# Kernel tuning notes

Measured on AMD Instinct MI355X. Metric: run time of the kernel, lower is better.

The kernel has to match this reference:

```python
import jax, jax.numpy as jnp
import numpy as np

C = 192          # filter_channels (= in_channels in this module)
K = 3            # kernel_size
NB = 10          # num_bins of rational-quadratic spline (VITS default)
TB = 5.0         # tail_bound
NF = 4           # number of ConvFlow steps per branch
L = 3            # DDSConv n_layers
LOG2PI = float(np.log(2.0 * np.pi))


def conv1x1(x, w, b):
    # x: (B, Cin, T), w: (Cout, Cin)
    return jnp.einsum('oi,bit->bot', w, x) + b[None, :, None]


def depthwise(x, w, b, dil):
    # x: (B, C, T), w: (C, 1, K), dilated depthwise conv, 'same' padding
    pad = dil * (K - 1) // 2
    y = jax.lax.conv_general_dilated(
        x, w, window_strides=(1,), padding=[(pad, pad)], rhs_dilation=(dil,),
        dimension_numbers=('NCH', 'OIH', 'NCH'), feature_group_count=x.shape[1])
    return y + b[None, :, None]


def layer_norm_c(x, g, b, eps=1e-5):
    # VITS LayerNorm: normalize over the channel axis (axis=1)
    m = jnp.mean(x, axis=1, keepdims=True)
    v = jnp.mean((x - m) ** 2, axis=1, keepdims=True)
    return (x - m) * jax.lax.rsqrt(v + eps) * g[None, :, None] + b[None, :, None]


def dds(x, x_mask, g, dep_w, dep_b, pw_w, pw_b, ln_g, ln_b):
    # DDSConv: dilated depth-separable conv stack with residual
    if g is not None:
        x = x + g
    for i in range(L):
        dil = K ** i
        y = depthwise(x * x_mask, dep_w[i], dep_b[i], dil)
        y = jax.nn.gelu(layer_norm_c(y, ln_g[i, 0], ln_b[i, 0]))
        y = conv1x1(y, pw_w[i], pw_b[i])
        y = jax.nn.gelu(layer_norm_c(y, ln_g[i, 1], ln_b[i, 1]))
        x = x + y  # dropout disabled in deterministic reference
    return x * x_mask


def ew_affine(z, x_mask, m, logs):
    y = (m[None, :, None] + jnp.exp(logs)[None, :, None] * z) * x_mask
    ld = jnp.sum(logs[None, :, None] * x_mask, axis=(1, 2))
    return y, ld


def rqs_forward(x_in, uw, uh, ud):
    # unconstrained rational-quadratic spline, forward direction, linear tails
    mb = 1e-3  # min bin width / height / derivative
    const = float(np.log(np.expm1(1.0 - mb)))
    inside = (x_in >= -TB) & (x_in <= TB)
    ud = jnp.pad(ud, ((0, 0), (0, 0), (0, 0), (1, 1)), constant_values=const)
    wd = jax.nn.softmax(uw, -1); wd = mb + (1.0 - mb * NB) * wd
    cw = jnp.cumsum(wd, -1)
    cw = jnp.concatenate([jnp.zeros_like(cw[..., :1]), cw], -1)
    cw = 2.0 * TB * cw - TB
    cw = cw.at[..., 0].set(-TB).at[..., -1].set(TB)
    wd = cw[..., 1:] - cw[..., :-1]
    ht = jax.nn.softmax(uh, -1); ht = mb + (1.0 - mb * NB) * ht
    ch = jnp.cumsum(ht, -1)
    ch = jnp.concatenate([jnp.zeros_like(ch[..., :1]), ch], -1)
    ch = 2.0 * TB * ch - TB
    ch = ch.at[..., 0].set(-TB).at[..., -1].set(TB)
    ht = ch[..., 1:] - ch[..., :-1]
    dv = mb + jax.nn.softplus(ud)  # (..., NB+1)
    xc = jnp.clip(x_in, -TB, TB)
    idx = jnp.clip(jnp.sum((xc[..., None] >= cw[..., :-1]).astype(jnp.int32), -1) - 1, 0, NB - 1)
    g = lambda a, i: jnp.take_along_axis(a, i[..., None], -1)[..., 0]
    icw, iw, ich, ih = g(cw, idx), g(wd, idx), g(ch, idx), g(ht, idx)
    idelta = ih / iw
    d0, d1 = g(dv, idx), g(dv, idx + 1)
    th = (xc - icw) / iw
    t1m = th * (1.0 - th)
    den = idelta + (d0 + d1 - 2.0 * idelta) * t1m
    out = ich + ih * (idelta * th * th + d0 * t1m) / den
    dnum = idelta * idelta * (d1 * th * th + 2.0 * idelta * t1m + d0 * (1.0 - th) ** 2)
    lad = jnp.log(dnum) - 2.0 * jnp.log(den)
    return jnp.where(inside, out, x_in), jnp.where(inside, lad, 0.0)


def conv_flow(z, x_mask, g, pre_w, pre_b, dep_w, dep_b, pw_w, pw_b, ln_g, ln_b, proj_w, proj_b):
    x0, x1 = z[:, :1], z[:, 1:]  # (B,1,T) each
    h = conv1x1(x0, pre_w, pre_b)
    h = dds(h, x_mask, g, dep_w, dep_b, pw_w, pw_b, ln_g, ln_b)
    h = conv1x1(h, proj_w, proj_b) * x_mask      # (B, 3*NB-1, T)
    B, _, T = h.shape
    h = h.reshape(B, 1, 3 * NB - 1, T).transpose(0, 1, 3, 2)  # (B,1,T,3*NB-1)
    s = 1.0 / np.sqrt(C)
    x1n, lad = rqs_forward(x1, h[..., :NB] * s, h[..., NB:2 * NB] * s, h[..., 2 * NB:])
    zo = jnp.concatenate([x0, x1n], 1) * x_mask
    return zo, jnp.sum(lad * x_mask, axis=(1, 2))


def _forward(x, x_mask, w, e_q, pre_w, pre_b, proj_w, proj_b,
             dds_dep_w, dds_dep_b, dds_pw_w, dds_pw_b, dds_ln_g, dds_ln_b,
             post_pre_w, post_pre_b, post_proj_w, post_proj_b,
             pdds_dep_w, pdds_dep_b, pdds_pw_w, pdds_pw_b, pdds_ln_g, pdds_ln_b,
             aff_m, aff_logs,
             f_pre_w, f_pre_b, f_dep_w, f_dep_b, f_pw_w, f_pw_b, f_ln_g, f_ln_b, f_proj_w, f_proj_b,
             paff_m, paff_logs,
             p_pre_w, p_pre_b, p_dep_w, p_dep_b, p_pw_w, p_pw_b, p_ln_g, p_ln_b, p_proj_w, p_proj_b):
    x = jax.lax.stop_gradient(x)
    h = conv1x1(x, pre_w, pre_b)
    h = dds(h, x_mask, None, dds_dep_w, dds_dep_b, dds_pw_w, dds_pw_b, dds_ln_g, dds_ln_b)
    h = conv1x1(h, proj_w, proj_b) * x_mask
    hw = conv1x1(w, post_pre_w, post_pre_b)
    hw = dds(hw, x_mask, None, pdds_dep_w, pdds_dep_b, pdds_pw_w, pdds_pw_b, pdds_ln_g, pdds_ln_b)
    hw = conv1x1(hw, post_proj_w, post_proj_b) * x_mask
    e = e_q * x_mask
    zq, ldq = ew_affine(e, x_mask, paff_m, paff_logs)
    gp = h + hw
    for i in range(NF):
        zq, ld = conv_flow(zq, x_mask, gp, p_pre_w[i], p_pre_b[i], p_dep_w[i], p_dep_b[i],
                           p_pw_w[i], p_pw_b[i], p_ln_g[i], p_ln_b[i], p_proj_w[i], p_proj_b[i])
        ldq = ldq + ld
        zq = zq[:, ::-1]  # Flip (logdet 0)
    zu, z1 = zq[:, :1], zq[:, 1:]
    u = jax.nn.sigmoid(zu) * x_mask
    z0 = (w - u) * x_mask
    ldq = ldq + jnp.sum((jax.nn.log_sigmoid(zu) + jax.nn.log_sigmoid(-zu)) * x_mask, axis=(1, 2))
    logq = jnp.sum(-0.5 * (LOG2PI + e * e) * x_mask, axis=(1, 2)) - ldq
    y0 = jnp.log(jnp.maximum(z0, 1e-5)) * x_mask  # Log flow
    ldt = jnp.sum(-y0, axis=(1, 2))
    z = jnp.concatenate([y0, z1], 1)
    z, ld = ew_affine(z, x_mask, aff_m, aff_logs)
    ldt = ldt + ld
    for i in range(NF):
        z, ld = conv_flow(z, x_mask, h, f_pre_w[i], f_pre_b[i], f_dep_w[i], f_dep_b[i],
                          f_pw_w[i], f_pw_b[i], f_ln_g[i], f_ln_b[i], f_proj_w[i], f_proj_b[i])
        ldt = ldt + ld
        z = z[:, ::-1]
    nll = jnp.sum(0.5 * (LOG2PI + z * z) * x_mask, axis=(1, 2)) - ldt
    return nll + logq  # (B,)


def setup_inputs() -> dict:
    key = jax.random.key(0)
    ks = jax.random.split(key, 24)
    B, T = 32, 768
    P = 3 * NB - 1
    r = lambda k, shape, s=0.05: jax.random.normal(k, shape, jnp.float32) * s
    d = {}
    d['x'] = jax.random.normal(ks[0], (B, C, T), jnp.float32)
    d['x_mask'] = jnp.ones((B, 1, T), jnp.float32)
    d['w'] = jax.random.uniform(ks[1], (B, 1, T), jnp.float32) * 10.0 + 1.0  # positive durations
    d['e_q'] = jax.random.normal(ks[2], (B, 2, T), jnp.float32)
    d['pre_w'] = r(ks[3], (C, C)); d['pre_b'] = jnp.zeros((C,), jnp.float32)
    d['proj_w'] = r(ks[4], (C, C)); d['proj_b'] = jnp.zeros((C,), jnp.float32)
    d['dds_dep_w'] = r(ks[5], (L, C, 1, K)); d['dds_dep_b'] = jnp.zeros((L, C), jnp.float32)
    d['dds_pw_w'] = r(ks[6], (L, C, C)); d['dds_pw_b'] = jnp.zeros((L, C), jnp.float32)
    d['dds_ln_g'] = jnp.ones((L, 2, C), jnp.float32); d['dds_ln_b'] = jnp.zeros((L, 2, C), jnp.float32)
    d['post_pre_w'] = r(ks[7], (C, 1)); d['post_pre_b'] = jnp.zeros((C,), jnp.float32)
    d['post_proj_w'] = r(ks[8], (C, C)); d['post_proj_b'] = jnp.zeros((C,), jnp.float32)
    d['pdds_dep_w'] = r(ks[9], (L, C, 1, K)); d['pdds_dep_b'] = jnp.zeros((L, C), jnp.float32)
    d['pdds_pw_w'] = r(ks[10], (L, C, C)); d['pdds_pw_b'] = jnp.zeros((L, C), jnp.float32)
    d['pdds_ln_g'] = jnp.ones((L, 2, C), jnp.float32); d['pdds_ln_b'] = jnp.zeros((L, 2, C), jnp.float32)
    d['aff_m'] = r(ks[11], (2,)); d['aff_logs'] = r(ks[12], (2,))
    d['f_pre_w'] = r(ks[13], (NF, C, 1)); d['f_pre_b'] = jnp.zeros((NF, C), jnp.float32)
    d['f_dep_w'] = r(ks[14], (NF, L, C, 1, K)); d['f_dep_b'] = jnp.zeros((NF, L, C), jnp.float32)
    d['f_pw_w'] = r(ks[15], (NF, L, C, C)); d['f_pw_b'] = jnp.zeros((NF, L, C), jnp.float32)
    d['f_ln_g'] = jnp.ones((NF, L, 2, C), jnp.float32); d['f_ln_b'] = jnp.zeros((NF, L, 2, C), jnp.float32)
    d['f_proj_w'] = r(ks[16], (NF, P, C), 0.01); d['f_proj_b'] = jnp.zeros((NF, P), jnp.float32)
    d['paff_m'] = r(ks[17], (2,)); d['paff_logs'] = r(ks[18], (2,))
    d['p_pre_w'] = r(ks[19], (NF, C, 1)); d['p_pre_b'] = jnp.zeros((NF, C), jnp.float32)
    d['p_dep_w'] = r(ks[20], (NF, L, C, 1, K)); d['p_dep_b'] = jnp.zeros((NF, L, C), jnp.float32)
    d['p_pw_w'] = r(ks[21], (NF, L, C, C)); d['p_pw_b'] = jnp.zeros((NF, L, C), jnp.float32)
    d['p_ln_g'] = jnp.ones((NF, L, 2, C), jnp.float32); d['p_ln_b'] = jnp.zeros((NF, L, 2, C), jnp.float32)
    d['p_proj_w'] = r(ks[22], (NF, P, C), 0.01); d['p_proj_b'] = jnp.zeros((NF, P), jnp.float32)
    return d


def reference(x, x_mask, w, e_q, pre_w, pre_b, proj_w, proj_b,
              dds_dep_w, dds_dep_b, dds_pw_w, dds_pw_b, dds_ln_g, dds_ln_b,
              post_pre_w, post_pre_b, post_proj_w, post_proj_b,
              pdds_dep_w, pdds_dep_b, pdds_pw_w, pdds_pw_b, pdds_ln_g, pdds_ln_b,
              aff_m, aff_logs,
              f_pre_w, f_pre_b, f_dep_w, f_dep_b, f_pw_w, f_pw_b, f_ln_g, f_ln_b, f_proj_w, f_proj_b,
              paff_m, paff_logs,
              p_pre_w, p_pre_b, p_dep_w, p_dep_b, p_pw_w, p_pw_b, p_ln_g, p_ln_b, p_proj_w, p_proj_b):
    return _forward(x, x_mask, w, e_q, pre_w, pre_b, proj_w, proj_b,
                    dds_dep_w, dds_dep_b, dds_pw_w, dds_pw_b, dds_ln_g, dds_ln_b,
                    post_pre_w, post_pre_b, post_proj_w, post_proj_b,
                    pdds_dep_w, pdds_dep_b, pdds_pw_w, pdds_pw_b, pdds_ln_g, pdds_ln_b,
                    aff_m, aff_logs,
                    f_pre_w, f_pre_b, f_dep_w, f_dep_b, f_pw_w, f_pw_b, f_ln_g, f_ln_b, f_proj_w, f_proj_b,
                    paff_m, paff_logs,
                    p_pre_w, p_pre_b, p_dep_w, p_dep_b, p_pw_w, p_pw_b, p_ln_g, p_ln_b, p_proj_w, p_proj_b)
```

## Files before the change

kernel.cpp:

```cpp
#include <hip/hip_runtime.h>
#include <math.h>

#define CC 192
#define TTT 768
#define PP 29
#define LOG2PI_F 1.8378770664093453f
#define WSLOT 36864
#define PSW 6144
#define XS 200
#define XSP 200
#define PARL 1728

typedef __attribute__((ext_vector_type(8))) short short8;
typedef __attribute__((ext_vector_type(4))) float floatx4;
typedef __attribute__((ext_vector_type(2))) float float2v;
union Frag { int4 i; short8 s; };

__device__ __forceinline__ float2v fma2(float2v a, float2v b, float2v c){
  return __builtin_elementwise_fma(a, b, c);
}
__device__ __forceinline__ float geluf(float x){
  float u = 1.5957691216057308f * (x + 0.044715f*x*x*x);
  return x * __builtin_amdgcn_rcpf(1.f + __expf(-u));
}
__device__ __forceinline__ float softplus_f(float x){
  return (x > 20.f) ? x : log1pf(__expf(x));
}
__device__ __forceinline__ float logsig_f(float x){
  return -softplus_f(-x);
}
__device__ __forceinline__ unsigned short f2bf(float f){
  unsigned int u = __builtin_bit_cast(unsigned int, f);
  u += 0x7fffu + ((u >> 16) & 1u);
  return (unsigned short)(u >> 16);
}
__device__ __forceinline__ unsigned int packbf2(float a0, float a1){
  return (unsigned int)f2bf(a0) | ((unsigned int)f2bf(a1) << 16);
}
__device__ __forceinline__ void unbf2(unsigned int u, float& lo, float& hi){
  lo = __builtin_bit_cast(float, u << 16);
  hi = __builtin_bit_cast(float, u & 0xffff0000u);
}
__device__ __forceinline__ float2v unbf2v(unsigned int u){
  float2v r;
  r.x = __builtin_bit_cast(float, u << 16);
  r.y = __builtin_bit_cast(float, u & 0xffff0000u);
  return r;
}
__device__ __forceinline__ void unp8(int4 v, float* o){
  unsigned int* p = (unsigned int*)&v;
  unbf2(p[0], o[0], o[1]); unbf2(p[1], o[2], o[3]);
  unbf2(p[2], o[4], o[5]); unbf2(p[3], o[6], o[7]);
}
__device__ __forceinline__ void f4arr(float4 v, float* o){ o[0]=v.x;o[1]=v.y;o[2]=v.z;o[3]=v.w; }
__device__ __forceinline__ float2v pick2(float4 a, float4 b, int p){
  switch(p){
    case 0: return (float2v){a.x, a.y};
    case 1: return (float2v){a.z, a.w};
    case 2: return (float2v){b.x, b.y};
    default: return (float2v){b.z, b.w};
  }
}

__global__ __launch_bounds__(256) void convert_w_k(
    const float* __restrict__ p0, const float* __restrict__ p1,
    const float* __restrict__ p2, const float* __restrict__ p3,
    const float* __restrict__ p4, const float* __restrict__ p5,
    const float* __restrict__ p6, const float* __restrict__ p7,
    const float* __restrict__ p8, unsigned short* __restrict__ Wb){
  int i = blockIdx.x*256 + threadIdx.x;
  const int totalA = 33*WSLOT;
  const int total = totalA + 8*PSW;
  if (i >= total) return;
  if (i < totalA){
    int slot = i / WSLOT, j = i % WSLOT;
    int e = j & 7, lane = (j>>3) & 63, kt = j >> 9;
    int k = kt % 6, tile = kt / 6;
    int co = tile*16 + (lane & 15);
    int kk = k*32 + (lane>>4)*8 + e;
    int r = co*CC + kk;
    const float* src;
    if      (slot == 0) src = p0 + r;
    else if (slot == 1) src = p1 + r;
    else if (slot == 2) src = p2 + r;
    else if (slot < 6)  src = p3 + (size_t)(slot-3)*WSLOT + r;
    else if (slot < 9)  src = p4 + (size_t)(slot-6)*WSLOT + r;
    else if (slot < 21) src = p5 + (size_t)(slot-9)*WSLOT + r;
    else                src = p6 + (size_t)(slot-21)*WSLOT + r;
    Wb[i] = f2bf(*src);
  } else {
    int r2 = i - totalA;
    int ps = r2 / PSW, j = r2 % PSW;
    int e = j & 7, lane = (j>>3) & 63, kt = j >> 9;
    int k = kt % 6, tile = kt / 6;
    int co = tile*16 + (lane & 15); if (co > PP-1) co = PP-1;
    int kk = k*32 + (lane>>4)*8 + e;
    const float* base = (ps < 4) ? (p7 + (size_t)ps*PP*CC) : (p8 + (size_t)(ps-4)*PP*CC);
    Wb[i] = f2bf(base[co*CC + kk]);
  }
}

__global__ __launch_bounds__(256) void pack_par_k(
    const float* __restrict__ dds_dep_w, const float* __restrict__ dds_dep_b,
    const float* __restrict__ dds_ln_g,  const float* __restrict__ dds_ln_b,
    const float* __restrict__ dds_pw_b,
    const float* __restrict__ pdds_dep_w, const float* __restrict__ pdds_dep_b,
    const float* __restrict__ pdds_ln_g,  const float* __restrict__ pdds_ln_b,
    const float* __restrict__ pdds_pw_b,
    const float* __restrict__ p_dep_w, const float* __restrict__ p_dep_b,
    const float* __restrict__ p_ln_g,  const float* __restrict__ p_ln_b,
    const float* __restrict__ p_pw_b,
    const float* __restrict__ f_dep_w, const float* __restrict__ f_dep_b,
    const float* __restrict__ f_ln_g,  const float* __restrict__ f_ln_b,
    const float* __restrict__ f_pw_b,
    float* __restrict__ P){
  int i = blockIdx.x*256 + threadIdx.x;
  const int total = 30*PARL;
  if (i >= total) return;
  int ls = i / PARL, r = i % PARL;
  int arr = r / 192, c = r % 192;
  const float *dep_w, *dep_b, *ln_g, *ln_b, *pw_b;
  int l;
  if (ls < 3){
    l = ls; dep_w = dds_dep_w; dep_b = dds_dep_b; ln_g = dds_ln_g; ln_b = dds_ln_b; pw_b = dds_pw_b;
  } else if (ls < 6){
    l = ls-3; dep_w = pdds_dep_w; dep_b = pdds_dep_b; ln_g = pdds_ln_g; ln_b = pdds_ln_b; pw_b = pdds_pw_b;
  } else if (ls < 18){
    int f = (ls-6)/3; l = (ls-6)%3;
    dep_w = p_dep_w + (size_t)f*3*CC*3; dep_b = p_dep_b + (size_t)f*3*CC;
    ln_g = p_ln_g + (size_t)f*3*2*CC;  ln_b = p_ln_b + (size_t)f*3*2*CC;
    pw_b = p_pw_b + (size_t)f*3*CC;
  } else {
    int f = (ls-18)/3; l = (ls-18)%3;
    dep_w = f_dep_w + (size_t)f*3*CC*3; dep_b = f_dep_b + (size_t)f*3*CC;
    ln_g = f_ln_g + (size_t)f*3*2*CC;  ln_b = f_ln_b + (size_t)f*3*2*CC;
    pw_b = f_pw_b + (size_t)f*3*CC;
  }
  float v;
  if      (arr < 3)  v = dep_w[((size_t)l*CC + c)*3 + arr];
  else if (arr == 3) v = dep_b[(size_t)l*CC + c];
  else if (arr == 4) v = ln_g[((size_t)l*2+0)*CC + c];
  else if (arr == 5) v = ln_b[((size_t)l*2+0)*CC + c];
  else if (arr == 6) v = ln_g[((size_t)l*2+1)*CC + c];
  else if (arr == 7) v = ln_b[((size_t)l*2+1)*CC + c];
  else               v = pw_b[(size_t)l*CC + c];
  P[i] = v;
}

__global__ __launch_bounds__(256) void trans_conv_k(
    const float* __restrict__ x, const unsigned short* __restrict__ Wsw,
    const float* __restrict__ bias, unsigned short* __restrict__ outb){
  __shared__ unsigned short bufX[32*XS];
  int b = blockIdx.y, t0 = blockIdx.x*32, tid = threadIdx.x;
  int tl4 = (tid & 7)*4, cr = tid >> 3;
  #pragma unroll
  for (int rnd=0; rnd<6; rnd++){
    int c = rnd*32 + cr;
    float4 v4 = *(const float4*)(x + ((size_t)b*CC + c)*TTT + t0 + tl4);
    bufX[(tl4+0)*XS + c] = f2bf(v4.x);
    bufX[(tl4+1)*XS + c] = f2bf(v4.y);
    bufX[(tl4+2)*XS + c] = f2bf(v4.z);
    bufX[(tl4+3)*XS + c] = f2bf(v4.w);
  }
  __syncthreads();
  int w = tid >> 6, lane = tid & 63;
  int n16 = lane & 15, quad = lane >> 4;
  Frag af[3][6];
  #pragma unroll
  for (int ct=0; ct<3; ct++){
    int tile = w*3 + ct;
    #pragma unroll
    for (int k=0;k<6;k++)
      af[ct][k].i = *(const int4*)(Wsw + ((size_t)(tile*6 + k)*64 + lane)*8);
  }
  floatx4 acc[3][2];
  #pragma unroll
  for (int ct=0;ct<3;ct++)
    #pragma unroll
    for (int tt=0;tt<2;tt++)
      acc[ct][tt] = (floatx4){0.f,0.f,0.f,0.f};
  #pragma unroll
  for (int k=0;k<6;k++){
    Frag bf[2];
    #pragma unroll
    for (int tt=0;tt<2;tt++)
      bf[tt].i = *(const int4*)&bufX[(tt*16+n16)*XS + k*32 + quad*8];
    #pragma unroll
    for (int ct=0;ct<3;ct++)
      #pragma unroll
      for (int tt=0;tt<2;tt++)
        acc[ct][tt] = __builtin_amdgcn_mfma_f32_16x16x32_bf16(af[ct][k].s, bf[tt].s, acc[ct][tt], 0,0,0);
  }
  __syncthreads();
  #pragma unroll
  for (int ct=0;ct<3;ct++){
    int cobase = w*48 + ct*16 + quad*4;
    float4 b4 = *(const float4*)(bias + cobase);
    #pragma unroll
    for (int tt=0;tt<2;tt++){
      int t = tt*16 + n16;
      uint2 wv;
      wv.x = packbf2(acc[ct][tt][0] + b4.x, acc[ct][tt][1] + b4.y);
      wv.y = packbf2(acc[ct][tt][2] + b4.z, acc[ct][tt][3] + b4.w);
      *(uint2*)&bufX[t*XS + cobase] = wv;
    }
  }
  __syncthreads();
  #pragma unroll
  for (int k=0;k<3;k++){
    int task = k*256 + tid;
    int row = task/24, cn = task%24;
    *(int4*)(outb + ((size_t)b*TTT + t0 + row)*CC + cn*8) = *(const int4*)&bufX[row*XS + cn*8];
  }
}

template<int DIL, int SPLITF>
__device__ __forceinline__ void dds_layer(
    unsigned short* __restrict__ ping,
    const float* __restrict__ pl,
    float* __restrict__ pnd, const float* __restrict__ pns,
    const float* __restrict__ mrow,
    float (* __restrict__ sqx)[2][2],
    const unsigned short* __restrict__ WL,
    int tid, int w, int lane, int n16, int quad, int row){
  constexpr int NT = SPLITF ? 6 : 12;
  const int tb = SPLITF ? ((w & 1)*6) : 0;
  const int rowL = SPLITF ? (16 + (w>>1)*16 + n16) : row;
  Frag bfr[6];
  floatx4 acc[NT];
  {
    int iL = rowL - DIL; iL = iL < 0 ? 0 : iL;
    int iR = rowL + DIL; iR = iR > 63 ? 63 : iR;
    float2v vv[24];
    float2v s2v = {0.f,0.f}, q2v = {0.f,0.f};
    #pragma unroll
    for (int j=0;j<6;j++){
      int kk = j*32 + quad*8;
      int4 L4 = *(const int4*)&ping[iL*XSP + kk];
      int4 C4 = *(const int4*)&ping[rowL*XSP + kk];
      int4 R4 = *(const int4*)&ping[iR*XSP + kk];
      unsigned int* Lp = (unsigned int*)&L4;
      unsigned int* Cp = (unsigned int*)&C4;
      unsigned int* Rp = (unsigned int*)&R4;
      float4 w0a = *(const float4*)&pl[kk],       w0b = *(const float4*)&pl[kk+4];
      float4 w1a = *(const float4*)&pl[192+kk],   w1b = *(const float4*)&pl[192+kk+4];
      float4 w2a = *(const float4*)&pl[384+kk],   w2b = *(const float4*)&pl[384+kk+4];
      float4 dba = *(const float4*)&pl[576+kk],   dbb = *(const float4*)&pl[576+kk+4];
      #pragma unroll
      for (int p=0;p<4;p++){
        float2v val = fma2(pick2(w0a,w0b,p), unbf2v(Lp[p]),
                      fma2(pick2(w1a,w1b,p), unbf2v(Cp[p]),
                      fma2(pick2(w2a,w2b,p), unbf2v(Rp[p]), pick2(dba,dbb,p))));
        vv[j*4+p] = val;
        s2v += val;
        q2v = fma2(val, val, q2v);
      }
    }
    float s = s2v.x + s2v.y, q = q2v.x + q2v.y;
    s += __shfl_xor(s, 16); s += __shfl_xor(s, 32);
    q += __shfl_xor(q, 16); q += __shfl_xor(q, 32);
    float mm = s*(1.f/CC);
    float rr = rsqrtf(q*(1.f/CC) - mm*mm + 1e-5f);
    float2v mm2 = {mm,mm}, rr2 = {rr,rr};
    #pragma unroll
    for (int j=0;j<6;j++){
      int kk = j*32 + quad*8;
      float4 g0a = *(const float4*)&pl[768+kk], g0b = *(const float4*)&pl[768+kk+4];
      float4 b0a = *(const float4*)&pl[960+kk], b0b = *(const float4*)&pl[960+kk+4];
      unsigned int wwp[4];
      #pragma unroll
      for (int p=0;p<4;p++){
        float2v a = fma2((vv[j*4+p]-mm2)*rr2, pick2(g0a,g0b,p), pick2(b0a,b0b,p));
        wwp[p] = packbf2(geluf(a.x), geluf(a.y));
      }
      bfr[j].i = make_int4((int)wwp[0], (int)wwp[1], (int)wwp[2], (int)wwp[3]);
    }
  }
  __syncthreads();
  if (pns){
    #pragma unroll
    for (int k=0;k<7;k++){
      int i2 = k*256 + tid;
      if (i2 < PARL) pnd[i2] = pns[i2];
    }
  }
  {
    Frag afb[2][6];
    #pragma unroll
    for (int k=0;k<6;k++)
      afb[0][k].i = *(const int4*)(WL + ((size_t)((tb+0)*6 + k)*64 + lane)*8);
    #pragma unroll
    for (int tile=0; tile<NT; tile++){
      int cur = tile & 1, nxt = cur ^ 1;
      if (tile < NT-1){
        #pragma unroll
        for (int k=0;k<6;k++)
          afb[nxt][k].i = *(const int4*)(WL + ((size_t)((tb+tile+1)*6 + k)*64 + lane)*8);
      }
      acc[tile] = (floatx4){0.f,0.f,0.f,0.f};
      #pragma unroll
      for (int k=0;k<6;k++)
        acc[tile] = __builtin_amdgcn_mfma_f32_16x16x32_bf16(afb[cur][k].s, bfr[k].s, acc[tile], 0,0,0);
    }
  }
  float2v s2p = {0.f,0.f}, q2p = {0.f,0.f};
  #pragma unroll
  for (int tile=0; tile<NT; tile++){
    int co = (tb+tile)*16 + quad*4;
    float4 pbv = *(const float4*)&pl[1536+co];
    acc[tile][0] += pbv.x; acc[tile][1] += pbv.y;
    acc[tile][2] += pbv.z; acc[tile][3] += pbv.w;
    float2v v01 = {acc[tile][0], acc[tile][1]};
    float2v v23 = {acc[tile][2], acc[tile][3]};
    s2p += v01 + v23;
    q2p = fma2(v01, v01, q2p);
    q2p = fma2(v23, v23, q2p);
  }
  float s2 = s2p.x + s2p.y, q2 = q2p.x + q2p.y;
  s2 += __shfl_xor(s2, 16); s2 += __shfl_xor(s2, 32);
  q2 += __shfl_xor(q2, 16); q2 += __shfl_xor(q2, 32);
  if constexpr (SPLITF){
    int r16 = rowL - 16;
    if (quad == 0){ sqx[r16][w&1][0] = s2; sqx[r16][w&1][1] = q2; }
    __syncthreads();
    int oh = (w&1)^1;
    s2 += sqx[r16][oh][0];
    q2 += sqx[r16][oh][1];
  }
  float cmP = s2*(1.f/CC);
  float crP = rsqrtf(q2*(1.f/CC) - cmP*cmP + 1e-5f);
  float mc = mrow[rowL];
  float2v mc2 = {mc,mc};
  float2v cm2 = {cmP,cmP}, cr2 = {crP,crP};
  #pragma unroll
  for (int tile=0; tile<NT; tile++){
    int co = (tb+tile)*16 + quad*4;
    float4 g1v = *(const float4*)&pl[1152+co];
    float4 b1v = *(const float4*)&pl[1344+co];
    uint2 ux = *(uint2*)&ping[rowL*XSP + co];
    float2v x01 = unbf2v(ux.x), x23 = unbf2v(ux.y);
    float2v v01 = {acc[tile][0], acc[tile][1]};
    float2v v23 = {acc[tile][2], acc[tile][3]};
    float2v a01 = fma2((v01-cm2)*cr2, (float2v){g1v.x,g1v.y}, (float2v){b1v.x,b1v.y});
    float2v a23 = fma2((v23-cm2)*cr2, (float2v){g1v.z,g1v.w}, (float2v){b1v.z,b1v.w});
    float2v h01 = (x01 + (float2v){geluf(a01.x), geluf(a01.y)}) * mc2;
    float2v h23 = (x23 + (float2v){geluf(a23.x), geluf(a23.y)}) * mc2;
    uint2 wv;
    wv.x = packbf2(h01.x, h01.y);
    wv.y = packbf2(h23.x, h23.y);
    *(uint2*)&ping[rowL*XSP + co] = wv;
  }
  __syncthreads();
}

__global__ __launch_bounds__(256,3) void mega_dds_k(
    const unsigned short* __restrict__ in,
    const float* __restrict__ zsrc, int zstride,
    const unsigned short* __restrict__ g,
    const float* __restrict__ mask,
    const float* __restrict__ parP,
    const float* __restrict__ pw1, const float* __restrict__ pb1,
    const unsigned short* __restrict__ Wsw,
    int srcmode, int outmode,
    const unsigned short* __restrict__ projW, const float* __restrict__ projB,
    float* __restrict__ z, int zs, float* __restrict__ acco,
    const unsigned short* __restrict__ cvW, const float* __restrict__ cvB,
    const unsigned short* __restrict__ addsrc, unsigned short* __restrict__ cvout,
    int cvmode){
  __shared__ unsigned short ping[64*XSP];
  __shared__ float par[2][PARL];
  __shared__ float mrow[64];
  __shared__ float sqx[32][2][2];
  float* pro = par[0];

  int b = blockIdx.y, t0 = blockIdx.x*32, tid = threadIdx.x;
  int ws0 = t0 - 16;
  int w = tid >> 6, lane = tid & 63;
  int n16 = lane & 15, quad = lane >> 4;
  int row = w*16 + n16;
  const float* mkb = mask + (size_t)b*TTT;

  if (tid < 64){
    int gt = ws0 + tid;
    bool inr = (gt >= 0) && (gt < TTT);
    int gc = gt < 0 ? 0 : (gt > TTT-1 ? TTT-1 : gt);
    mrow[tid] = inr ? mkb[gc] : 0.f;
  }
  #pragma unroll
  for (int k=0;k<7;k++){
    int i2 = k*256 + tid;
    if (i2 < PARL) par[0][i2] = parP[i2];
  }
  if (srcmode == 0){
    #pragma unroll
    for (int k=0;k<6;k++){
      int task = k*256 + tid;
      int r = task/24, cn = task%24, c0 = cn*8;
      int gt = ws0 + r;
      bool inr = (gt >= 0) && (gt < TTT);
      int gc = gt < 0 ? 0 : (gt > TTT-1 ? TTT-1 : gt);
      float mv = inr ? mkb[gc] : 0.f;
      float hv[8];
      unp8(*(const int4*)(in + ((size_t)b*TTT + gc)*CC + c0), hv);
      int4 pk;
      pk.x = (int)packbf2(hv[0]*mv, hv[1]*mv); pk.y = (int)packbf2(hv[2]*mv, hv[3]*mv);
      pk.z = (int)packbf2(hv[4]*mv, hv[5]*mv); pk.w = (int)packbf2(hv[6]*mv, hv[7]*mv);
      *(int4*)&ping[r*XSP + c0] = pk;
    }
  } else {
    #pragma unroll
    for (int k=0;k<6;k++){
      int task = k*256 + tid;
      int r = task/24, cn = task%24, c0 = cn*8;
      int gt = ws0 + r;
      bool inr = (gt >= 0) && (gt < TTT);
      int gc = gt < 0 ? 0 : (gt > TTT-1 ? TTT-1 : gt);
      float mv = inr ? mkb[gc] : 0.f;
      float zv = inr ? zsrc[(size_t)b*zstride + gc] : 0.f;
      float hv[8];
      if (g){
        unp8(*(const int4*)(g + ((size_t)b*TTT + gc)*CC + c0), hv);
      } else {
        #pragma unroll
        for (int e=0;e<8;e++) hv[e] = 0.f;
      }
      float4 pwa = *(const float4*)(pw1 + c0);
      float4 pwb2 = *(const float4*)(pw1 + c0 + 4);
      float4 pba = *(const float4*)(pb1 + c0);
      float4 pbb2 = *(const float4*)(pb1 + c0 + 4);
      float pwv[8], pbv[8];
      f4arr(pwa, pwv); f4arr(pwb2, pwv+4);
      f4arr(pba, pbv); f4arr(pbb2, pbv+4);
      float ov[8];
      #pragma unroll
      for (int e=0;e<8;e++) ov[e] = (hv[e] + fmaf(pwv[e], zv, pbv[e]))*mv;
      int4 pk;
      pk.x = (int)packbf2(ov[0], ov[1]); pk.y = (int)packbf2(ov[2], ov[3]);
      pk.z = (int)packbf2(ov[4], ov[5]); pk.w = (int)packbf2(ov[6], ov[7]);
      *(int4*)&ping[r*XSP + c0] = pk;
    }
  }
  __syncthreads();

  dds_layer<1,0>(ping, par[0], par[1], parP + (size_t)1*PARL, mrow, sqx,
                 Wsw + 0*(size_t)WSLOT, tid, w, lane, n16, quad, row);
  dds_layer<3,0>(ping, par[1], par[0], parP + (size_t)2*PARL, mrow, sqx,
                 Wsw + 1*(size_t)WSLOT, tid, w, lane, n16, quad, row);
  dds_layer<9,1>(ping, par[0], nullptr, nullptr, mrow, sqx,
                 Wsw + 2*(size_t)WSLOT, tid, w, lane, n16, quad, row);

  if (outmode == 2){
    if (cvmode == 2){
      #pragma unroll
      for (int k=0;k<3;k++){
        int task = k*256 + tid;
        int r = task/24, cn = task%24;
        int dr = r + ((r >= 16) ? 32 : 0);
        *(int4*)&ping[dr*XSP + cn*8] =
            *(const int4*)(addsrc + ((size_t)b*TTT + t0 + r)*CC + cn*8);
      }
    }
    Frag af[3][6];
    #pragma unroll
    for (int ct=0; ct<3; ct++){
      int tile = w*3 + ct;
      #pragma unroll
      for (int k=0;k<6;k++)
        af[ct][k].i = *(const int4*)(cvW + ((size_t)(tile*6 + k)*64 + lane)*8);
    }
    floatx4 acc2[3][2];
    #pragma unroll
    for (int ct=0;ct<3;ct++)
      #pragma unroll
      for (int tt=0;tt<2;tt++)
        acc2[ct][tt] = (floatx4){0.f,0.f,0.f,0.f};
    #pragma unroll
    for (int k=0;k<6;k++){
      Frag bf[2];
      #pragma unroll
      for (int tt=0;tt<2;tt++)
        bf[tt].i = *(const int4*)&ping[(16 + tt*16 + n16)*XSP + k*32 + quad*8];
      #pragma unroll
      for (int ct=0;ct<3;ct++)
        #pragma unroll
        for (int tt=0;tt<2;tt++)
          acc2[ct][tt] = __builtin_amdgcn_mfma_f32_16x16x32_bf16(af[ct][k].s, bf[tt].s, acc2[ct][tt], 0,0,0);
    }
    __syncthreads();
    #pragma unroll
    for (int ct=0;ct<3;ct++){
      int cobase = w*48 + ct*16 + quad*4;
      float4 b4 = *(const float4*)(cvB + cobase);
      float ba[4] = {b4.x, b4.y, b4.z, b4.w};
      #pragma unroll
      for (int tt=0;tt<2;tt++){
        int t = tt*16 + n16;
        float mv = mrow[16 + t];
        float av[4] = {0.f,0.f,0.f,0.f};
        if (cvmode == 2){
          int hr = t + ((t >= 16) ? 32 : 0);
          uint2 uy = *(uint2*)&ping[hr*XSP + cobase];
          unbf2(uy.x, av[0], av[1]); unbf2(uy.y, av[2], av[3]);
        }
        float hh[4];
        #pragma unroll
        for (int r=0;r<4;r++){
          float v = (acc2[ct][tt][r] + ba[r]) * mv;
          if (cvmode == 2) v += av[r];
          hh[r] = v;
        }
        uint2 wv; wv.x = packbf2(hh[0], hh[1]); wv.y = packbf2(hh[2], hh[3]);
        *(uint2*)&ping[(16 + t)*XSP + cobase] = wv;
      }
    }
    __syncthreads();
    #pragma unroll
    for (int k=0;k<3;k++){
      int task = k*256 + tid;
      int r = task/24, cn = task%24, c0 = cn*8;
      *(int4*)(cvout + ((size_t)b*TTT + t0 + r)*CC + c0) = *(const int4*)&ping[(16+r)*XSP + c0];
    }
    return;
  }

  {
    int ctp = w & 1;
    int prow = 16 + (w>>1)*16 + n16;
    Frag afp[6];
    #pragma unroll
    for (int k=0;k<6;k++)
      afp[k].i = *(const int4*)(projW + ((size_t)(ctp*6 + k)*64 + lane)*8);
    Frag bfp[6];
    #pragma unroll
    for (int k=0;k<6;k++)
      bfp[k].i = *(const int4*)&ping[prow*XSP + k*32 + quad*8];
    floatx4 acc2 = (floatx4){0.f,0.f,0.f,0.f};
    #pragma unroll
    for (int k=0;k<6;k++)
      acc2 = __builtin_amdgcn_mfma_f32_16x16x32_bf16(afp[k].s, bfp[k].s, acc2, 0,0,0);
    int rt = prow - 16;
    float mv = mrow[prow];
    #pragma unroll
    for (int r=0;r<4;r++){
      int co = ctp*16 + quad*4 + r;
      if (co < PP) pro[rt*30 + co] = (acc2[r] + projB[co]) * mv;
    }
  }
  __syncthreads();
  if (tid < 32){
    const float scv = 0.07216878364870323f;
    int tg = t0 + tid;
    float m = mrow[16+tid];
    float* z0p = z + ((size_t)b*2 + zs)*TTT + tg;
    float* z1p = z + ((size_t)b*2 + (1-zs))*TTT + tg;
    float xs = *z1p;
    float uw[10], uh[10], ud[9];
    #pragma unroll
    for (int k=0;k<10;k++) uw[k]=pro[tid*30+k]*scv;
    #pragma unroll
    for (int k=0;k<10;k++) uh[k]=pro[tid*30+10+k]*scv;
    #pragma unroll
    for (int k=0;k<9;k++)  ud[k]=pro[tid*30+20+k];
    bool inside = (xs >= -5.f) && (xs <= 5.f);
    float xc = fminf(fmaxf(xs,-5.f),5.f);
    float mx=uw[0];
    #pragma unroll
    for (int k=1;k<10;k++) mx=fmaxf(mx,uw[k]);
    float sw=0.f; float wd[10];
    #pragma unroll
    for (int k=0;k<10;k++){ wd[k]=__expf(uw[k]-mx); sw+=wd[k]; }
    float invw = 1.f/sw;
    #pragma unroll
    for (int k=0;k<10;k++) wd[k]=fmaf(0.99f*invw, wd[k], 1e-3f);
    float mh=uh[0];
    #pragma unroll
    for (int k=1;k<10;k++) mh=fmaxf(mh,uh[k]);
    float sh=0.f; float ht[10];
    #pragma unroll
    for (int k=0;k<10;k++){ ht[k]=__expf(uh[k]-mh); sh+=ht[k]; }
    float invh = 1.f/sh;
    #pragma unroll
    for (int k=0;k<10;k++) ht[k]=fmaf(0.99f*invh, ht[k], 1e-3f);
    float cw=-5.f, icw=-5.f, iw=1.f; int idx=0;
    #pragma unroll
    for (int i2=0;i2<10;i2++){
      float nw = (i2==9) ? 5.f : fmaf(10.f, wd[i2], cw);
      if (cw <= xc){ idx=i2; icw=cw; iw=nw-cw; }
      cw=nw;
    }
    float ch=-5.f, ich=-5.f, ih=1.f;
    #pragma unroll
    for (int i2=0;i2<10;i2++){
      float nh = (i2==9) ? 5.f : fmaf(10.f, ht[i2], ch);
      if (i2==idx){ ich=ch; ih=nh-ch; }
      ch=nh;
    }
    const float UDC = logf(expm1f(0.999f));
    float d0=1.f, d1=1.f;
    #pragma unroll
    for (int k=0;k<11;k++){
      float uu = (k==0 || k==10) ? UDC : ud[k-1];
      float dk = 1e-3f + softplus_f(uu);
      if (k==idx)   d0=dk;
      if (k==idx+1) d1=dk;
    }
    float idel = ih/iw;
    float th = (xc-icw)/iw;
    float t1m = th*(1.f-th);
    float den = idel + (d0+d1-2.f*idel)*t1m;
    float outv = ich + ih*(idel*th*th + d0*t1m)/den;
    float omt = 1.f-th;
    float dnum = idel*idel*(d1*th*th + 2.f*idel*t1m + d0*omt*omt);
    float lad = logf(dnum) - 2.f*logf(den);
    float y = inside ? outv : xs;
    lad = inside ? lad : 0.f;
    *z1p = y*m;
    *z0p = (*z0p)*m;
    float lm = lad*m;
    lm += __shfl_xor(lm, 1); lm += __shfl_xor(lm, 2);
    lm += __shfl_xor(lm, 4); lm += __shfl_xor(lm, 8);
    lm += __shfl_xor(lm, 16);
    if (tid == 0) atomicAdd(acco + b, -lm);
  }
}

__global__ __launch_bounds__(256) void init_z_k(
    const float* __restrict__ e_q, const float* __restrict__ mask,
    const float* __restrict__ pm, const float* __restrict__ pl,
    float* __restrict__ z, float* __restrict__ acc){
  __shared__ float red[256];
  int b = blockIdx.y; int t = blockIdx.x*256 + threadIdx.x;
  float m = mask[(size_t)b*TTT + t];
  float pl0=pl[0], pl1=pl[1];
  float e0 = e_q[((size_t)b*2+0)*TTT + t]*m;
  float e1 = e_q[((size_t)b*2+1)*TTT + t]*m;
  z[((size_t)b*2+0)*TTT + t] = fmaf(__expf(pl0), e0, pm[0])*m;
  z[((size_t)b*2+1)*TTT + t] = fmaf(__expf(pl1), e1, pm[1])*m;
  float contrib = -0.5f*(LOG2PI_F + e0*e0)*m - 0.5f*(LOG2PI_F + e1*e1)*m - (pl0+pl1)*m;
  int tid = threadIdx.x;
  red[tid] = contrib;
  __syncthreads();
  for (int o=128;o>0;o>>=1){ if (tid<o) red[tid]+=red[tid+o]; __syncthreads(); }
  if (tid==0) atomicAdd(acc+b, red[0]);
}

__global__ __launch_bounds__(256) void final_pre_k(
    float* __restrict__ z, const float* __restrict__ w_in, const float* __restrict__ mask,
    const float* __restrict__ am, const float* __restrict__ al, float* __restrict__ acc){
  __shared__ float red[256];
  int b = blockIdx.y; int t = blockIdx.x*256 + threadIdx.x;
  float m = mask[(size_t)b*TTT + t];
  float zu  = z[((size_t)b*2+0)*TTT + t];
  float z1v = z[((size_t)b*2+1)*TTT + t];
  float wv  = w_in[(size_t)b*TTT + t];
  float u  = m / (1.f + __expf(-zu));
  float z0 = (wv - u)*m;
  float y0 = logf(fmaxf(z0, 1e-5f))*m;
  float al0=al[0], al1=al[1];
  z[((size_t)b*2+0)*TTT + t] = fmaf(__expf(al0), y0,  am[0])*m;
  z[((size_t)b*2+1)*TTT + t] = fmaf(__expf(al1), z1v, am[1])*m;
  float contrib = -(logsig_f(zu)+logsig_f(-zu))*m + y0 - (al0+al1)*m;
  int tid = threadIdx.x;
  red[tid] = contrib;
  __syncthreads();
  for (int o=128;o>0;o>>=1){ if (tid<o) red[tid]+=red[tid+o]; __syncthreads(); }
  if (tid==0) atomicAdd(acc+b, red[0]);
}

__global__ __launch_bounds__(256) void final_post_k(
    const float* __restrict__ z, const float* __restrict__ mask, float* __restrict__ acc){
  __shared__ float red[256];
  int b = blockIdx.y; int t = blockIdx.x*256 + threadIdx.x;
  float m = mask[(size_t)b*TTT + t];
  float z0 = z[((size_t)b*2+0)*TTT + t];
  float z1 = z[((size_t)b*2+1)*TTT + t];
  float contrib = 0.5f*(LOG2PI_F + z0*z0)*m + 0.5f*(LOG2PI_F + z1*z1)*m;
  int tid = threadIdx.x;
  red[tid] = contrib;
  __syncthreads();
  for (int o=128;o>0;o>>=1){ if (tid<o) red[tid]+=red[tid+o]; __syncthreads(); }
  if (tid==0) atomicAdd(acc+b, red[0]);
}

__global__ void write_out_k(const float* __restrict__ acc, float* __restrict__ out, int n){
  int i = threadIdx.x;
  if (i < n) out[i] = acc[i];
}

extern "C" void kernel_launch(void* const* d_in, const int* in_sizes, int n_in,
                              void* d_out, int out_size, void* d_ws, size_t ws_size,
                              hipStream_t stream){
  (void)n_in; (void)out_size; (void)ws_size;
  const float* x         = (const float*)d_in[0];
  const float* mask      = (const float*)d_in[1];
  const float* w_in      = (const float*)d_in[2];
  const float* e_q       = (const float*)d_in[3];
  const float* pre_w     = (const float*)d_in[4];
  const float* pre_b     = (const float*)d_in[5];
  const float* proj_w    = (const float*)d_in[6];
  const float* proj_b    = (const float*)d_in[7];
  const float* dds_dep_w = (const float*)d_in[8];
  const float* dds_dep_b = (const float*)d_in[9];
  const float* dds_pw_w  = (const float*)d_in[10];
  const float* dds_pw_b  = (const float*)d_in[11];
  const float* dds_ln_g  = (const float*)d_in[12];
  const float* dds_ln_b  = (const float*)d_in[13];
  const float* post_pre_w  = (const float*)d_in[14];
  const float* post_pre_b  = (const float*)d_in[15];
  const float* post_proj_w = (const float*)d_in[16];
  const float* post_proj_b = (const float*)d_in[17];
  const float* pdds_dep_w  = (const float*)d_in[18];
  const float* pdds_dep_b  = (const float*)d_in[19];
  const float* pdds_pw_w   = (const float*)d_in[20];
  const float* pdds_pw_b   = (const float*)d_in[21];
  const float* pdds_ln_g   = (const float*)d_in[22];
  const float* pdds_ln_b   = (const float*)d_in[23];
  const float* aff_m    = (const float*)d_in[24];
  const float* aff_logs = (const float*)d_in[25];
  const float* f_pre_w  = (const float*)d_in[26];
  const float* f_pre_b  = (const float*)d_in[27];
  const float* f_dep_w  = (const float*)d_in[28];
  const float* f_dep_b  = (const float*)d_in[29];
  const float* f_pw_w   = (const float*)d_in[30];
  const float* f_pw_b   = (const float*)d_in[31];
  const float* f_ln_g   = (const float*)d_in[32];
  const float* f_ln_b   = (const float*)d_in[33];
  const float* f_proj_w = (const float*)d_in[34];
  const float* f_proj_b = (const float*)d_in[35];
  const float* paff_m    = (const float*)d_in[36];
  const float* paff_logs = (const float*)d_in[37];
  const float* p_pre_w  = (const float*)d_in[38];
  const float* p_pre_b  = (const float*)d_in[39];
  const float* p_dep_w  = (const float*)d_in[40];
  const float* p_dep_b  = (const float*)d_in[41];
  const float* p_pw_w   = (const float*)d_in[42];
  const float* p_pw_b   = (const float*)d_in[43];
  const float* p_ln_g   = (const float*)d_in[44];
  const float* p_ln_b   = (const float*)d_in[45];
  const float* p_proj_w = (const float*)d_in[46];
  const float* p_proj_b = (const float*)d_in[47];

  int Bn = in_sizes[0] / (CC*TTT);
  size_t big2 = (size_t)Bn*CC*TTT;
  unsigned short* xT = (unsigned short*)d_ws;
  unsigned short* A  = xT + big2;
  unsigned short* Bb = A  + big2;
  unsigned short* H  = Bb + big2;
  unsigned short* GP = H  + big2;
  unsigned short* Wb = GP + big2;
  size_t wtot = 33*(size_t)WSLOT + 8*(size_t)PSW;
  float* parP = (float*)(Wb + ((wtot + 7) & ~(size_t)7));
  float* zbuf = parP + 30*(size_t)PARL;
  float* acc  = zbuf + (size_t)Bn*2*TTT;

  hipMemsetAsync(acc, 0, Bn*sizeof(float), stream);
  convert_w_k<<<(int)((wtot + 255)/256), 256, 0, stream>>>(
      pre_w, proj_w, post_proj_w, dds_pw_w, pdds_pw_w, p_pw_w, f_pw_w,
      p_proj_w, f_proj_w, Wb);
  pack_par_k<<<(30*PARL + 255)/256, 256, 0, stream>>>(
      dds_dep_w, dds_dep_b, dds_ln_g, dds_ln_b, dds_pw_b,
      pdds_dep_w, pdds_dep_b, pdds_ln_g, pdds_ln_b, pdds_pw_b,
      p_dep_w, p_dep_b, p_ln_g, p_ln_b, p_pw_b,
      f_dep_w, f_dep_b, f_ln_g, f_ln_b, f_pw_b, parP);

  dim3 g32(TTT/32, Bn), g256(TTT/256, Bn);
  dim3 b256(256);

  unsigned short* W_pre      = Wb + 0*(size_t)WSLOT;
  unsigned short* W_proj     = Wb + 1*(size_t)WSLOT;
  unsigned short* W_postproj = Wb + 2*(size_t)WSLOT;
  unsigned short* W_dds      = Wb + 3*(size_t)WSLOT;
  unsigned short* W_pdds     = Wb + 6*(size_t)WSLOT;
  unsigned short* W_ppw      = Wb + 9*(size_t)WSLOT;
  unsigned short* W_fpw      = Wb + 21*(size_t)WSLOT;
  unsigned short* W_pproj    = Wb + 33*(size_t)WSLOT;
  unsigned short* W_fproj    = W_pproj + 4*(size_t)PSW;

  trans_conv_k<<<g32, b256, 0, stream>>>(x, W_pre, pre_b, A);
  mega_dds_k<<<g32, b256, 0, stream>>>(A, nullptr, 0, nullptr, mask,
      parP + 0*(size_t)3*PARL, nullptr, nullptr,
      W_dds, 0, 2, nullptr, nullptr, nullptr, 0, acc,
      W_proj, proj_b, nullptr, H, 1);

  mega_dds_k<<<g32, b256, 0, stream>>>(nullptr, w_in, TTT, nullptr, mask,
      parP + 1*(size_t)3*PARL, post_pre_w, post_pre_b,
      W_pdds, 1, 2, nullptr, nullptr, nullptr, 0, acc,
      W_postproj, post_proj_b, H, GP, 2);

  init_z_k<<<g256, b256, 0, stream>>>(e_q, mask, paff_m, paff_logs, zbuf, acc);

  for (int f=0; f<4; f++){
    int s = f & 1;
    mega_dds_k<<<g32, b256, 0, stream>>>(nullptr, zbuf + (size_t)s*TTT, 2*TTT, GP, mask,
        parP + (size_t)(2+f)*3*PARL,
        p_pre_w + (size_t)f*CC, p_pre_b + (size_t)f*CC,
        W_ppw + (size_t)f*3*WSLOT, 1, 1,
        W_pproj + (size_t)f*PSW, p_proj_b + (size_t)f*PP, zbuf, s, acc,
        nullptr, nullptr, nullptr, nullptr, 0);
  }

  final_pre_k<<<g256, b256, 0, stream>>>(zbuf, w_in, mask, aff_m, aff_logs, acc);

  for (int f=0; f<4; f++){
    int s = f & 1;
    mega_dds_k<<<g32, b256, 0, stream>>>(nullptr, zbuf + (size_t)s*TTT, 2*TTT, H, mask,
        parP + (size_t)(6+f)*3*PARL,
        f_pre_w + (size_t)f*CC, f_pre_b + (size_t)f*CC,
        W_fpw + (size_t)f*3*WSLOT, 1, 1,
        W_fproj + (size_t)f*PSW, f_proj_b + (size_t)f*PP, zbuf, s, acc,
        nullptr, nullptr, nullptr, nullptr, 0);
  }

  final_post_k<<<g256, b256, 0, stream>>>(zbuf, mask, acc);
  write_out_k<<<1, 64, 0, stream>>>(acc, (float*)d_out, Bn);
}
```

Measured before the change: 741.9 us.

## Fuse init/final elementwise kernels into flow kernels, prefetch weights two tiles ahead

Removes the separate init_z, final_pre and final_post kernels. Their elementwise affine transforms and log-likelihood contributions now run inside the first and last ConvFlow mega kernels through new pmode and finmode flags, which cuts three launches and their global round trips. It also swaps the bf16 pack for a hardware v_cvt_pk_bf16_f32 instruction and changes the MFMA A-fragment double buffer to load two tiles ahead. The cost is extra branching and recomputation of the affine prologue in the halo rows, plus some register pressure from the added state.

Result: faster. 680.4 us (-8.3%).

```diff
diff --git a/kernel.cpp b/kernel.cpp
--- a/kernel.cpp
+++ b/kernel.cpp
@@ -35,7 +35,9 @@
   return (unsigned short)(u >> 16);
 }
 __device__ __forceinline__ unsigned int packbf2(float a0, float a1){
-  return (unsigned int)f2bf(a0) | ((unsigned int)f2bf(a1) << 16);
+  unsigned int r;
+  asm("v_cvt_pk_bf16_f32 %0, %1, %2" : "=v"(r) : "v"(a0), "v"(a1));
+  return r;
 }
 __device__ __forceinline__ void unbf2(unsigned int u, float& lo, float& hi){
   lo = __builtin_bit_cast(float, u << 16);
@@ -290,17 +292,20 @@
     for (int k=0;k<6;k++)
       afb[0][k].i = *(const int4*)(WL + ((size_t)((tb+0)*6 + k)*64 + lane)*8);
     #pragma unroll
+    for (int k=0;k<6;k++)
+      afb[1][k].i = *(const int4*)(WL + ((size_t)((tb+1)*6 + k)*64 + lane)*8);
+    #pragma unroll
     for (int tile=0; tile<NT; tile++){
-      int cur = tile & 1, nxt = cur ^ 1;
-      if (tile < NT-1){
+      int cur = tile & 1;
+      acc[tile] = (floatx4){0.f,0.f,0.f,0.f};
+      #pragma unroll
+      for (int k=0;k<6;k++)
+        acc[tile] = __builtin_amdgcn_mfma_f32_16x16x32_bf16(afb[cur][k].s, bfr[k].s, acc[tile], 0,0,0);
+      if (tile < NT-2){
         #pragma unroll
         for (int k=0;k<6;k++)
-          afb[nxt][k].i = *(const int4*)(WL + ((size_t)((tb+tile+1)*6 + k)*64 + lane)*8);
+          afb[cur][k].i = *(const int4*)(WL + ((size_t)((tb+tile+2)*6 + k)*64 + lane)*8);
       }
-      acc[tile] = (floatx4){0.f,0.f,0.f,0.f};
-      #pragma unroll
-      for (int k=0;k<6;k++)
-        acc[tile] = __builtin_amdgcn_mfma_f32_16x16x32_bf16(afb[cur][k].s, bfr[k].s, acc[tile], 0,0,0);
     }
   }
   float2v s2p = {0.f,0.f}, q2p = {0.f,0.f};
@@ -366,7 +371,9 @@
     float* __restrict__ z, int zs, float* __restrict__ acco,
     const unsigned short* __restrict__ cvW, const float* __restrict__ cvB,
     const unsigned short* __restrict__ addsrc, unsigned short* __restrict__ cvout,
-    int cvmode){
+    int cvmode,
+    int pmode, int finmode, const float* __restrict__ aux,
+    const float* __restrict__ pmv, const float* __restrict__ plv){
   __shared__ unsigned short ping[64*XSP];
   __shared__ float par[2][PARL];
   __shared__ float mrow[64];
@@ -379,6 +386,12 @@
   int n16 = lane & 15, quad = lane >> 4;
   int row = w*16 + n16;
   const float* mkb = mask + (size_t)b*TTT;
+
+  float pm0=0.f, pm1=0.f, lg0=0.f, lg1=0.f, ex0=0.f, ex1=0.f;
+  if (pmode){
+    pm0 = pmv[0]; pm1 = pmv[1]; lg0 = plv[0]; lg1 = plv[1];
+    ex0 = __expf(lg0); ex1 = __expf(lg1);
+  }
 
   if (tid < 64){
     int gt = ws0 + tid;
@@ -416,7 +429,19 @@
       bool inr = (gt >= 0) && (gt < TTT);
       int gc = gt < 0 ? 0 : (gt > TTT-1 ? TTT-1 : gt);
       float mv = inr ? mkb[gc] : 0.f;
-      float zv = inr ? zsrc[(size_t)b*zstride + gc] : 0.f;
+      float zv;
+      if (pmode == 1){
+        float e0 = aux[((size_t)b*2+0)*TTT + gc] * mv;
+        zv = fmaf(ex0, e0, pm0)*mv;
+      } else if (pmode == 2){
+        float zu = zsrc[(size_t)b*zstride + gc];
+        float wv = aux[(size_t)b*TTT + gc];
+        float u  = mv / (1.f + __expf(-zu));
+        float y0 = logf(fmaxf((wv - u)*mv, 1e-5f))*mv;
+        zv = fmaf(ex0, y0, pm0)*mv;
+      } else {
+        zv = inr ? zsrc[(size_t)b*zstride + gc] : 0.f;
+      }
       float hv[8];
       if (g){
         unp8(*(const int4*)(g + ((size_t)b*TTT + gc)*CC + c0), hv);
@@ -553,7 +578,28 @@
     float m = mrow[16+tid];
     float* z0p = z + ((size_t)b*2 + zs)*TTT + tg;
     float* z1p = z + ((size_t)b*2 + (1-zs))*TTT + tg;
-    float xs = *z1p;
+    float xs, zwr0, extra = 0.f;
+    if (pmode == 1){
+      float e0c = aux[((size_t)b*2+0)*TTT + tg]*m;
+      float e1c = aux[((size_t)b*2+1)*TTT + tg]*m;
+      zwr0 = fmaf(ex0, e0c, pm0)*m;
+      xs   = fmaf(ex1, e1c, pm1)*m;
+      extra = -0.5f*(LOG2PI_F + e0c*e0c)*m - 0.5f*(LOG2PI_F + e1c*e1c)*m - (lg0+lg1)*m;
+    } else if (pmode == 2){
+      xs = fmaf(ex1, *z1p, pm1)*m;
+      zwr0 = (*z0p)*m;
+    } else if (pmode == 3){
+      float zu = *z1p;
+      float wv = aux[(size_t)b*TTT + tg];
+      float u  = m/(1.f + __expf(-zu));
+      float y0 = logf(fmaxf((wv - u)*m, 1e-5f))*m;
+      xs = fmaf(ex0, y0, pm0)*m;
+      extra = -(logsig_f(zu)+logsig_f(-zu))*m + y0 - (lg0+lg1)*m;
+      zwr0 = (*z0p)*m;
+    } else {
+      xs = *z1p;
+      zwr0 = (*z0p)*m;
+    }
     float uw[10], uh[10], ud[9];
     #pragma unroll
     for (int k=0;k<10;k++) uw[k]=pro[tid*30+k]*scv;
@@ -614,72 +660,18 @@
     float lad = logf(dnum) - 2.f*logf(den);
     float y = inside ? outv : xs;
     lad = inside ? lad : 0.f;
-    *z1p = y*m;
-    *z0p = (*z0p)*m;
-    float lm = lad*m;
-    lm += __shfl_xor(lm, 1); lm += __shfl_xor(lm, 2);
-    lm += __shfl_xor(lm, 4); lm += __shfl_xor(lm, 8);
-    lm += __shfl_xor(lm, 16);
-    if (tid == 0) atomicAdd(acco + b, -lm);
-  }
-}
-
-__global__ __launch_bounds__(256) void init_z_k(
-    const float* __restrict__ e_q, const float* __restrict__ mask,
-    const float* __restrict__ pm, const float* __restrict__ pl,
-    float* __restrict__ z, float* __restrict__ acc){
-  __shared__ float red[256];
-  int b = blockIdx.y; int t = blockIdx.x*256 + threadIdx.x;
-  float m = mask[(size_t)b*TTT + t];
-  float pl0=pl[0], pl1=pl[1];
-  float e0 = e_q[((size_t)b*2+0)*TTT + t]*m;
-  float e1 = e_q[((size_t)b*2+1)*TTT + t]*m;
-  z[((size_t)b*2+0)*TTT + t] = fmaf(__expf(pl0), e0, pm[0])*m;
-  z[((size_t)b*2+1)*TTT + t] = fmaf(__expf(pl1), e1, pm[1])*m;
-  float contrib = -0.5f*(LOG2PI_F + e0*e0)*m - 0.5f*(LOG2PI_F + e1*e1)*m - (pl0+pl1)*m;
-  int tid = threadIdx.x;
-  red[tid] = contrib;
-  __syncthreads();
-  for (int o=128;o>0;o>>=1){ if (tid<o) red[tid]+=red[tid+o]; __syncthreads(); }
-  if (tid==0) atomicAdd(acc+b, red[0]);
-}
-
-__global__ __launch_bounds__(256) void final_pre_k(
-    float* __restrict__ z, const float* __restrict__ w_in, const float* __restrict__ mask,
-    const float* __restrict__ am, const float* __restrict__ al, float* __restrict__ acc){
-  __shared__ float red[256];
-  int b = blockIdx.y; int t = blockIdx.x*256 + threadIdx.x;
-  float m = mask[(size_t)b*TTT + t];
-  float zu  = z[((size_t)b*2+0)*TTT + t];
-  float z1v = z[((size_t)b*2+1)*TTT + t];
-  float wv  = w_in[(size_t)b*TTT + t];
-  float u  = m / (1.f + __expf(-zu));
-  float z0 = (wv - u)*m;
-  float y0 = logf(fmaxf(z0, 1e-5f))*m;
-  float al0=al[0], al1=al[1];
-  z[((size_t)b*2+0)*TTT + t] = fmaf(__expf(al0), y0,  am[0])*m;
-  z[((size_t)b*2+1)*TTT + t] = fmaf(__expf(al1), z1v, am[1])*m;
-  float contrib = -(logsig_f(zu)+logsig_f(-zu))*m + y0 - (al0+al1)*m;
-  int tid = threadIdx.x;
-  red[tid] = contrib;
-  __syncthreads();
-  for (int o=128;o>0;o>>=1){ if (tid<o) red[tid]+=red[tid+o]; __syncthreads(); }
-  if (tid==0) atomicAdd(acc+b, red[0]);
-}
-
-__global__ __launch_bounds__(256) void final_post_k(
-    const float* __restrict__ z, const float* __restrict__ mask, float* __restrict__ acc){
-  __shared__ float red[256];
-  int b = blockIdx.y; int t = blockIdx.x*256 + threadIdx.x;
-  float m = mask[(size_t)b*TTT + t];
-  float z0 = z[((size_t)b*2+0)*TTT + t];
-  float z1 = z[((size_t)b*2+1)*TTT + t];
-  float contrib = 0.5f*(LOG2PI_F + z0*z0)*m + 0.5f*(LOG2PI_F + z1*z1)*m;
-  int tid = threadIdx.x;
-  red[tid] = contrib;
-  __syncthreads();
-  for (int o=128;o>0;o>>=1){ if (tid<o) red[tid]+=red[tid+o]; __syncthreads(); }
-  if (tid==0) atomicAdd(acc+b, red[0]);
+    float y1 = y*m;
+    *z1p = y1;
+    *z0p = zwr0;
+    if (finmode){
+      extra += 0.5f*(LOG2PI_F + y1*y1)*m + 0.5f*(LOG2PI_F + zwr0*zwr0)*m;
+    }
+    float c = extra - lad*m;
+    c += __shfl_xor(c, 1); c += __shfl_xor(c, 2);
+    c += __shfl_xor(c, 4); c += __shfl_xor(c, 8);
+    c += __shfl_xor(c, 16);
+    if (tid == 0) atomicAdd(acco + b, c);
+  }
 }
 
 __global__ void write_out_k(const float* __restrict__ acc, float* __restrict__ out, int n){
@@ -763,7 +755,7 @@
       p_dep_w, p_dep_b, p_ln_g, p_ln_b, p_pw_b,
       f_dep_w, f_dep_b, f_ln_g, f_ln_b, f_pw_b, parP);
 
-  dim3 g32(TTT/32, Bn), g256(TTT/256, Bn);
+  dim3 g32(TTT/32, Bn);
   dim3 b256(256);
 
   unsigned short* W_pre      = Wb + 0*(size_t)WSLOT;
@@ -780,14 +772,14 @@
   mega_dds_k<<<g32, b256, 0, stream>>>(A, nullptr, 0, nullptr, mask,
       parP + 0*(size_t)3*PARL, nullptr, nullptr,
       W_dds, 0, 2, nullptr, nullptr, nullptr, 0, acc,
-      W_proj, proj_b, nullptr, H, 1);
+      W_proj, proj_b, nullptr, H, 1,
+      0, 0, nullptr, nullptr, nullptr);
 
   mega_dds_k<<<g32, b256, 0, stream>>>(nullptr, w_in, TTT, nullptr, mask,
       parP + 1*(size_t)3*PARL, post_pre_w, post_pre_b,
       W_pdds, 1, 2, nullptr, nullptr, nullptr, 0, acc,
-      W_postproj, post_proj_b, H, GP, 2);
-
-  init_z_k<<<g256, b256, 0, stream>>>(e_q, mask, paff_m, paff_logs, zbuf, acc);
+      W_postproj, post_proj_b, H, GP, 2,
+      0, 0, nullptr, nullptr, nullptr);
 
   for (int f=0; f<4; f++){
     int s = f & 1;
@@ -796,21 +788,21 @@
         p_pre_w + (size_t)f*CC, p_pre_b + (size_t)f*CC,
         W_ppw + (size_t)f*3*WSLOT, 1, 1,
         W_pproj + (size_t)f*PSW, p_proj_b + (size_t)f*PP, zbuf, s, acc,
-        nullptr, nullptr, nullptr, nullptr, 0);
-  }
-
-  final_pre_k<<<g256, b256, 0, stream>>>(zbuf, w_in, mask, aff_m, aff_logs, acc);
+        nullptr, nullptr, nullptr, nullptr, 0,
+        (f==0) ? 1 : 0, 0, e_q, paff_m, paff_logs);
+  }
 
   for (int f=0; f<4; f++){
     int s = f & 1;
+    int pmode = (f==0) ? 2 : ((f==1) ? 3 : 0);
     mega_dds_k<<<g32, b256, 0, stream>>>(nullptr, zbuf + (size_t)s*TTT, 2*TTT, H, mask,
         parP + (size_t)(6+f)*3*PARL,
         f_pre_w + (size_t)f*CC, f_pre_b + (size_t)f*CC,
         W_fpw + (size_t)f*3*WSLOT, 1, 1,
         W_fproj + (size_t)f*PSW, f_proj_b + (size_t)f*PP, zbuf, s, acc,
-        nullptr, nullptr, nullptr, nullptr, 0);
-  }
-
-  final_post_k<<<g256, b256, 0, stream>>>(zbuf, mask, acc);
+        nullptr, nullptr, nullptr, nullptr, 0,
+        pmode, (f==3) ? 1 : 0, w_in, aff_m, aff_logs);
+  }
+
   write_out_k<<<1, 64, 0, stream>>>(acc, (float*)d_out, Bn);
 }
```
